# Performance work log

Hardware: AMD Instinct MI355X
Metric: run time of the kernel (lower is better)

Reference implementation:

```python
import jax, jax.numpy as jnp
import numpy as np
from jax import lax

B, SEQ, D, DEPTH = 256, 50, 256, 4
N, K, R = 16, 4, 16  # d_state, d_conv, dt_rank
EPS = 1e-5


def rmsnorm(x, w):
    var = jnp.mean(jnp.square(x), axis=-1, keepdims=True)
    return x * lax.rsqrt(var + EPS) * w


def mamba_mixer(h, in_proj_w, conv_w, conv_b, x_proj_w, dt_proj_w, dt_proj_b, A_log, D_skip, out_proj_w):
    # h: (B, L, D)
    xz = h @ in_proj_w                       # (B, L, 2D)
    x_in, z = jnp.split(xz, 2, axis=-1)      # each (B, L, D)
    # causal depthwise conv1d, kernel K, groups=D
    x_bdl = x_in.transpose(0, 2, 1)          # (B, D, L)
    kern = conv_w[:, None, :]                # (D, 1, K)
    x_c = lax.conv_general_dilated(x_bdl, kern, window_strides=(1,),
                                   padding=[(K - 1, 0)], feature_group_count=D,
                                   dimension_numbers=('NCH', 'OIH', 'NCH'))
    x_c = jax.nn.silu(x_c + conv_b[None, :, None]).transpose(0, 2, 1)  # (B, L, D)
    # input-dependent SSM params
    x_dbl = x_c @ x_proj_w                   # (B, L, R+2N)
    dt = jax.nn.softplus(x_dbl[..., :R] @ dt_proj_w + dt_proj_b)       # (B, L, D)
    Bm = x_dbl[..., R:R + N]                 # (B, L, N)
    Cm = x_dbl[..., R + N:]                  # (B, L, N)
    A = -jnp.exp(A_log)                      # (D, N)
    dA = jnp.exp(dt[..., None] * A)          # (B, L, D, N)
    dBx = (dt * x_c)[..., None] * Bm[:, :, None, :]                    # (B, L, D, N)

    def step(hstate, inp):
        dA_t, dBx_t, C_t = inp
        hstate = dA_t * hstate + dBx_t      # (B, D, N)
        y_t = jnp.einsum('bdn,bn->bd', hstate, C_t)
        return hstate, y_t

    h0 = jnp.zeros((h.shape[0], D, N), dtype=h.dtype)
    xs = (dA.transpose(1, 0, 2, 3), dBx.transpose(1, 0, 2, 3), Cm.transpose(1, 0, 2))
    _, ys = lax.scan(step, h0, xs)           # (L, B, D)
    y = ys.transpose(1, 0, 2) + D_skip * x_c
    y = y * jax.nn.silu(z)
    return y @ out_proj_w                    # (B, L, D)


def setup_inputs() -> dict:
    key = jax.random.key(0)
    ks = jax.random.split(key, 16)
    sc = lambda *s: 0.02
    inp = {
        'x': jax.random.normal(ks[0], (B, SEQ), dtype=jnp.float32),
        'proj_w': jax.random.normal(ks[1], (1, D), dtype=jnp.float32) * 0.5,
        'proj_b': jnp.zeros((D,), dtype=jnp.float32),
        'cls_token': jax.random.normal(ks[2], (1, 1, D), dtype=jnp.float32) * 0.02,
        'pos_embed': jax.random.normal(ks[3], (1, SEQ + 1, D), dtype=jnp.float32) * 0.02,
        'norm_w': jnp.ones((DEPTH, D), dtype=jnp.float32),
        'in_proj_w': jax.random.normal(ks[4], (DEPTH, D, 2 * D), dtype=jnp.float32) * (D ** -0.5),
        'conv_w': jax.random.normal(ks[5], (DEPTH, D, K), dtype=jnp.float32) * 0.3,
        'conv_b': jnp.zeros((DEPTH, D), dtype=jnp.float32),
        'x_proj_w': jax.random.normal(ks[6], (DEPTH, D, R + 2 * N), dtype=jnp.float32) * (D ** -0.5),
        'dt_proj_w': jax.random.normal(ks[7], (DEPTH, R, D), dtype=jnp.float32) * (R ** -0.5),
        'dt_proj_b': jnp.log(jnp.expm1(jnp.full((DEPTH, D), 0.01, dtype=jnp.float32))),
        'A_log': jnp.broadcast_to(jnp.log(jnp.arange(1, N + 1, dtype=jnp.float32)), (DEPTH, D, N)).copy(),
        'D_skip': jnp.ones((DEPTH, D), dtype=jnp.float32),
        'out_proj_w': jax.random.normal(ks[8], (DEPTH, D, D), dtype=jnp.float32) * (D ** -0.5),
        'norm_f_w': jnp.ones((D,), dtype=jnp.float32),
    }
    return inp


def reference(x, proj_w, proj_b, cls_token, pos_embed, norm_w, in_proj_w, conv_w,
              conv_b, x_proj_w, dt_proj_w, dt_proj_b, A_log, D_skip, out_proj_w, norm_f_w):
    # LinearEmbed: (B, SEQ) -> (B, SEQ, 1) -> (B, SEQ, D)
    h = x[..., None] @ proj_w + proj_b
    h = h + pos_embed[:, :-1, :]
    cls = cls_token + pos_embed[:, -1:, :]
    h = jnp.concatenate([jnp.broadcast_to(cls, (h.shape[0], 1, D)), h], axis=1)  # (B, L=51, D)
    residual = None
    for i in range(DEPTH):
        residual = h if residual is None else residual + h
        hn = rmsnorm(residual, norm_w[i])
        h = mamba_mixer(hn, in_proj_w[i], conv_w[i], conv_b[i], x_proj_w[i],
                        dt_proj_w[i], dt_proj_b[i], A_log[i], D_skip[i], out_proj_w[i])
    out = rmsnorm(h, norm_f_w)
    return out[:, 0, :]  # return_type='cls'
```

## Files before the change

kernel.cpp:

```cpp
#include <hip/hip_runtime.h>
#include <math.h>

#define DD 256
#define DEPTH 4
#define XD 48


__global__ __launch_bounds__(256, 1)
void stageA(int L,
            const float* __restrict__ cls_token,
            const float* __restrict__ pos_embed,
            const float* __restrict__ norm_w,
            const float* __restrict__ in_proj_w,
            const float* __restrict__ conv_w,
            const float* __restrict__ conv_b,
            float* __restrict__ ws)
{
    const int tid = threadIdx.x, bid = blockIdx.x;
    float* xc_g = ws;
    float* zv_g = ws + DD;
    const float* hv_g = ws + 2*DD;
    float* res_e = ws + 3*DD;
    float* res_o = ws + 4*DD;

    __shared__ float hn[DD];
    __shared__ float4 part[64][4];
    __shared__ float red[4];
    __shared__ float rstd_s;

    float rn;
    if (L == 0) rn = cls_token[tid] + pos_embed[50*DD + tid];
    else        rn = ((L-1) & 1 ? res_o : res_e)[tid] + hv_g[tid];
    if (bid == 0) ((L & 1) ? res_o : res_e)[tid] = rn;

    float ss = rn * rn;
    #pragma unroll
    for (int o = 32; o > 0; o >>= 1) ss += __shfl_down(ss, o, 64);
    if ((tid & 63) == 0) red[tid >> 6] = ss;
    __syncthreads();
    if (tid == 0)
        rstd_s = rsqrtf((red[0]+red[1]+red[2]+red[3]) * (1.f/DD) + 1e-5f);
    __syncthreads();
    hn[tid] = rn * rstd_s * norm_w[L*DD + tid];
    __syncthreads();

    {
        const float4* W4 = (const float4*)in_proj_w + (size_t)L * DD * 128;
        const int c = tid & 3, seg = tid >> 2;
        const int col4 = bid*4 + c;
        float4 acc = make_float4(0.f, 0.f, 0.f, 0.f);
        #pragma unroll
        for (int i = 0; i < 4; ++i) {
            const int d = seg*4 + i;
            const float h = hn[d];
            const float4 w = W4[(size_t)d*128 + col4];
            acc.x += h*w.x; acc.y += h*w.y; acc.z += h*w.z; acc.w += h*w.w;
        }
        part[seg][c] = acc;
    }
    __syncthreads();
    #pragma unroll
    for (int off = 32; off >= 8; off >>= 1) {
        const int s = tid >> 2, c = tid & 3;
        if (s < off) {
            float4 a = part[s][c], b = part[s+off][c];
            a.x += b.x; a.y += b.y; a.z += b.z; a.w += b.w;
            part[s][c] = a;
        }
        __syncthreads();
    }
    if (tid < 16) {
        const int j = tid;
        float s = 0.f;
        #pragma unroll
        for (int g = 0; g < 8; ++g)
            s += ((const float*)&part[g][j >> 2])[j & 3];
        const int gc = bid*16 + j;
        if (gc < DD) {
            const float pre = conv_w[(L*DD + gc)*4 + 3]*s + conv_b[L*DD + gc];
            xc_g[gc] = pre / (1.f + __expf(-pre));
        } else {
            zv_g[gc - DD] = s;
        }
    }
}

__global__ __launch_bounds__(256, 1)
void stageB(int L,
            const float* __restrict__ x_proj_w,
            const float* __restrict__ dt_proj_w,
            const float* __restrict__ dt_proj_b,
            const float* __restrict__ D_skip,
            const float* __restrict__ out_proj_w,
            float* __restrict__ ws)
{
    const int tid = threadIdx.x, bid = blockIdx.x;
    const float* xc_g = ws;
    const float* zv_g = ws + DD;
    float* hv_g = ws + 2*DD;

    __shared__ float xcl[DD], yv[DD], xdbl[XD];
    __shared__ float xp[XD][4];
    __shared__ float4 part[64][4];

    xcl[tid] = xc_g[tid];
    const float zval = zv_g[tid];
    __syncthreads();

    if (tid < 192) {
        const int j = tid >> 2, q = tid & 3;
        const float* Wx = x_proj_w + (size_t)L * DD * XD;
        float acc = 0.f;
        #pragma unroll 8
        for (int i = 0; i < 64; ++i) {
            const int d = q*64 + i;
            acc += xcl[d] * Wx[(size_t)d*XD + j];
        }
        xp[j][q] = acc;
    }
    __syncthreads();
    if (tid < XD) xdbl[tid] = xp[tid][0] + xp[tid][1] + xp[tid][2] + xp[tid][3];
    __syncthreads();

    {
        const float* Wdt = dt_proj_w + (size_t)L * 16 * DD;
        float acc = dt_proj_b[L*DD + tid];
        #pragma unroll
        for (int r = 0; r < 16; ++r) acc += xdbl[r] * Wdt[r*DD + tid];
        const float dt = fmaxf(acc, 0.f) + log1pf(__expf(-fabsf(acc)));
        float sbc = 0.f;
        #pragma unroll
        for (int n = 0; n < 16; ++n) sbc += xdbl[16+n] * xdbl[32+n];
        const float y = (dt*sbc + D_skip[L*DD + tid]) * xcl[tid];
        yv[tid] = y * (zval / (1.f + __expf(-zval)));
    }
    __syncthreads();

    {
        const float4* Wo = (const float4*)out_proj_w + (size_t)L * DD * 64;
        const int c = tid & 3, seg = tid >> 2;
        const int col4 = bid*4 + c;
        float4 acc = make_float4(0.f, 0.f, 0.f, 0.f);
        #pragma unroll
        for (int i = 0; i < 4; ++i) {
            const int d = seg*4 + i;
            const float y = yv[d];
            const float4 w = Wo[(size_t)d*64 + col4];
            acc.x += y*w.x; acc.y += y*w.y; acc.z += y*w.z; acc.w += y*w.w;
        }
        part[seg][c] = acc;
    }
    __syncthreads();
    #pragma unroll
    for (int off = 32; off >= 8; off >>= 1) {
        const int s = tid >> 2, c = tid & 3;
        if (s < off) {
            float4 a = part[s][c], b = part[s+off][c];
            a.x += b.x; a.y += b.y; a.z += b.z; a.w += b.w;
            part[s][c] = a;
        }
        __syncthreads();
    }
    if (tid < 16) {
        const int j = tid;
        float s = 0.f;
        #pragma unroll
        for (int g = 0; g < 8; ++g)
            s += ((const float*)&part[g][j >> 2])[j & 3];
        hv_g[bid*16 + j] = s;
    }
}

__global__ __launch_bounds__(256, 1)
void finalK(const float* __restrict__ norm_f_w,
            const float* __restrict__ ws,
            float* __restrict__ out)
{
    const int tid = threadIdx.x, bid = blockIdx.x;
    const float* hv_g = ws + 2*DD;
    __shared__ float hn[DD];
    __shared__ float red[4];
    __shared__ float rstd_s;

    const float x = hv_g[tid];
    float ss = x * x;
    #pragma unroll
    for (int o = 32; o > 0; o >>= 1) ss += __shfl_down(ss, o, 64);
    if ((tid & 63) == 0) red[tid >> 6] = ss;
    __syncthreads();
    if (tid == 0)
        rstd_s = rsqrtf((red[0]+red[1]+red[2]+red[3]) * (1.f/DD) + 1e-5f);
    __syncthreads();
    hn[tid] = x * rstd_s * norm_f_w[tid];
    __syncthreads();

    const float4* o4 = (const float4*)hn;
    float4* out4 = (float4*)out;
    #pragma unroll
    for (int k = 0; k < 4; ++k) {
        const int idx = k*256 + tid;
        const int row = bid*16 + (idx >> 6);
        out4[(size_t)row*64 + (idx & 63)] = o4[idx & 63];
    }
}

extern "C" void kernel_launch(void* const* d_in, const int* in_sizes, int n_in,
                              void* d_out, int out_size, void* d_ws, size_t ws_size,
                              hipStream_t stream) {
    const float* cls_token  = (const float*)d_in[3];
    const float* pos_embed  = (const float*)d_in[4];
    const float* norm_w     = (const float*)d_in[5];
    const float* in_proj_w  = (const float*)d_in[6];
    const float* conv_w     = (const float*)d_in[7];
    const float* conv_b     = (const float*)d_in[8];
    const float* x_proj_w   = (const float*)d_in[9];
    const float* dt_proj_w  = (const float*)d_in[10];
    const float* dt_proj_b  = (const float*)d_in[11];
    const float* D_skip     = (const float*)d_in[13];
    const float* out_proj_w = (const float*)d_in[14];
    const float* norm_f_w   = (const float*)d_in[15];
    float* out = (float*)d_out;
    float* ws  = (float*)d_ws;

    for (int L = 0; L < DEPTH; ++L) {
        stageA<<<dim3(32), dim3(256), 0, stream>>>(
            L, cls_token, pos_embed, norm_w, in_proj_w, conv_w, conv_b, ws);
        stageB<<<dim3(16), dim3(256), 0, stream>>>(
            L, x_proj_w, dt_proj_w, dt_proj_b, D_skip, out_proj_w, ws);
    }
    finalK<<<dim3(16), dim3(256), 0, stream>>>(norm_f_w, ws, out);
}
```

Before: 38.12 us.

## Fuse all layer stages into one persistent kernel with grid barriers

Replaces the nine separate kernel launches (two per layer plus a final norm) with a single persistent 16-block kernel. A software grid barrier on an atomic counter separates the phases, and a tiny init kernel resets the counter. Intermediates pass between blocks through agent-scope atomic loads and stores, and the residual now stays in registers. The in_proj stage is retiled so 16 blocks each cover 32 columns. This removes per-launch overhead, but adds spin-barrier latency and relies on relaxed atomics without explicit fences for ordering.

```diff
diff --git a/kernel.cpp b/kernel.cpp
--- a/kernel.cpp
+++ b/kernel.cpp
@@ -4,229 +4,216 @@
 #define DD 256
 #define DEPTH 4
 #define XD 48
-
-
-__global__ __launch_bounds__(256, 1)
-void stageA(int L,
-            const float* __restrict__ cls_token,
-            const float* __restrict__ pos_embed,
-            const float* __restrict__ norm_w,
-            const float* __restrict__ in_proj_w,
-            const float* __restrict__ conv_w,
-            const float* __restrict__ conv_b,
-            float* __restrict__ ws)
+#define NBLK 16
+#define NTHR 256
+
+
+__device__ __forceinline__ float llc_loadf(const float* p) {
+    return __hip_atomic_load(p, __ATOMIC_RELAXED, __HIP_MEMORY_SCOPE_AGENT);
+}
+__device__ __forceinline__ void llc_storef(float* p, float v) {
+    __hip_atomic_store(p, v, __ATOMIC_RELAXED, __HIP_MEMORY_SCOPE_AGENT);
+}
+
+__device__ __forceinline__ void grid_bar(unsigned int* cnt, unsigned int target) {
+    __syncthreads();
+    if (threadIdx.x == 0) {
+        __hip_atomic_fetch_add(cnt, 1u, __ATOMIC_RELAXED, __HIP_MEMORY_SCOPE_AGENT);
+        while (__hip_atomic_load(cnt, __ATOMIC_RELAXED, __HIP_MEMORY_SCOPE_AGENT) < target)
+            __builtin_amdgcn_s_sleep(1);
+    }
+    __syncthreads();
+}
+
+__global__ void netmamba_init(unsigned int* cnt) { *cnt = 0u; }
+
+__global__ __launch_bounds__(NTHR, 1)
+void netmamba_persist(const float* __restrict__ cls_token,
+                      const float* __restrict__ pos_embed,
+                      const float* __restrict__ norm_w,
+                      const float* __restrict__ in_proj_w,
+                      const float* __restrict__ conv_w,
+                      const float* __restrict__ conv_b,
+                      const float* __restrict__ x_proj_w,
+                      const float* __restrict__ dt_proj_w,
+                      const float* __restrict__ dt_proj_b,
+                      const float* __restrict__ D_skip,
+                      const float* __restrict__ out_proj_w,
+                      const float* __restrict__ norm_f_w,
+                      float* __restrict__ out,
+                      float* __restrict__ ws)
 {
     const int tid = threadIdx.x, bid = blockIdx.x;
     float* xc_g = ws;
     float* zv_g = ws + DD;
-    const float* hv_g = ws + 2*DD;
-    float* res_e = ws + 3*DD;
-    float* res_o = ws + 4*DD;
-
-    __shared__ float hn[DD];
-    __shared__ float4 part[64][4];
+    float* hv_g = ws + 2 * DD;
+    unsigned int* cnt = (unsigned int*)(ws + 1024);
+
+    __shared__ float hn[DD], xcl[DD], yv[DD], xdbl[XD];
+    __shared__ float4 partA[32][8];
+    __shared__ float4 partB[64][4];
+    __shared__ float xp[XD][4];
     __shared__ float red[4];
     __shared__ float rstd_s;
 
-    float rn;
-    if (L == 0) rn = cls_token[tid] + pos_embed[50*DD + tid];
-    else        rn = ((L-1) & 1 ? res_o : res_e)[tid] + hv_g[tid];
-    if (bid == 0) ((L & 1) ? res_o : res_e)[tid] = rn;
-
-    float ss = rn * rn;
-    #pragma unroll
-    for (int o = 32; o > 0; o >>= 1) ss += __shfl_down(ss, o, 64);
-    if ((tid & 63) == 0) red[tid >> 6] = ss;
+    float res_reg = 0.f;
+    unsigned int phase = 0;
+
+    for (int L = 0; L < DEPTH; ++L) {
+        float rn;
+        if (L == 0) rn = cls_token[tid] + pos_embed[50 * DD + tid];
+        else        rn = res_reg + llc_loadf(&hv_g[tid]);
+        res_reg = rn;
+
+        float ss = rn * rn;
+        #pragma unroll
+        for (int o = 32; o > 0; o >>= 1) ss += __shfl_down(ss, o, 64);
+        if ((tid & 63) == 0) red[tid >> 6] = ss;
+        __syncthreads();
+        if (tid == 0)
+            rstd_s = rsqrtf((red[0] + red[1] + red[2] + red[3]) * (1.f / DD) + 1e-5f);
+        __syncthreads();
+        hn[tid] = rn * rstd_s * norm_w[L * DD + tid];
+        __syncthreads();
+
+        {
+            const float4* W4 = (const float4*)in_proj_w + (size_t)L * DD * 128;
+            const int cg = tid & 7, seg = tid >> 3;
+            const int col4 = bid * 8 + cg;
+            float4 acc = make_float4(0.f, 0.f, 0.f, 0.f);
+            #pragma unroll
+            for (int i = 0; i < 8; ++i) {
+                const int d = seg * 8 + i;
+                const float h = hn[d];
+                const float4 w = W4[(size_t)d * 128 + col4];
+                acc.x += h * w.x; acc.y += h * w.y;
+                acc.z += h * w.z; acc.w += h * w.w;
+            }
+            partA[seg][cg] = acc;
+        }
+        __syncthreads();
+        if (tid < 32) {
+            const float* pf = (const float*)partA;
+            float s = 0.f;
+            #pragma unroll
+            for (int g = 0; g < 32; ++g) s += pf[g * 32 + tid];
+            const int gc = bid * 32 + tid;
+            if (gc < DD) {
+                const float pre = conv_w[(L * DD + gc) * 4 + 3] * s + conv_b[L * DD + gc];
+                llc_storef(&xc_g[gc], pre / (1.f + __expf(-pre)));
+            } else {
+                llc_storef(&zv_g[gc - DD], s);
+            }
+        }
+        ++phase;
+        grid_bar(cnt, phase * NBLK);
+
+        xcl[tid] = llc_loadf(&xc_g[tid]);
+        const float zval = llc_loadf(&zv_g[tid]);
+        __syncthreads();
+
+        if (tid < 192) {
+            const int j = tid >> 2, q = tid & 3;
+            const float* Wx = x_proj_w + (size_t)L * DD * XD;
+            float acc = 0.f;
+            #pragma unroll 8
+            for (int i = 0; i < 64; ++i) {
+                const int d = q * 64 + i;
+                acc += xcl[d] * Wx[(size_t)d * XD + j];
+            }
+            xp[j][q] = acc;
+        }
+        __syncthreads();
+        if (tid < XD) xdbl[tid] = xp[tid][0] + xp[tid][1] + xp[tid][2] + xp[tid][3];
+        __syncthreads();
+
+        {
+            const float* Wdt = dt_proj_w + (size_t)L * 16 * DD;
+            float acc = dt_proj_b[L * DD + tid];
+            #pragma unroll
+            for (int r = 0; r < 16; ++r) acc += xdbl[r] * Wdt[r * DD + tid];
+            const float dtv = fmaxf(acc, 0.f) + log1pf(__expf(-fabsf(acc)));
+            float sbc = 0.f;
+            #pragma unroll
+            for (int n = 0; n < 16; ++n) sbc += xdbl[16 + n] * xdbl[32 + n];
+            const float y = (dtv * sbc + D_skip[L * DD + tid]) * xcl[tid];
+            yv[tid] = y * (zval / (1.f + __expf(-zval)));
+        }
+        __syncthreads();
+
+        {
+            const float4* Wo = (const float4*)out_proj_w + (size_t)L * DD * 64;
+            const int c = tid & 3, seg = tid >> 2;
+            const int col4 = bid * 4 + c;
+            float4 acc = make_float4(0.f, 0.f, 0.f, 0.f);
+            #pragma unroll
+            for (int i = 0; i < 4; ++i) {
+                const int d = seg * 4 + i;
+                const float y = yv[d];
+                const float4 w = Wo[(size_t)d * 64 + col4];
+                acc.x += y * w.x; acc.y += y * w.y;
+                acc.z += y * w.z; acc.w += y * w.w;
+            }
+            partB[seg][c] = acc;
+        }
+        __syncthreads();
+        #pragma unroll
+        for (int off = 32; off >= 8; off >>= 1) {
+            const int s = tid >> 2, c = tid & 3;
+            if (s < off) {
+                float4 a = partB[s][c], b = partB[s + off][c];
+                a.x += b.x; a.y += b.y; a.z += b.z; a.w += b.w;
+                partB[s][c] = a;
+            }
+            __syncthreads();
+        }
+        if (tid < 16) {
+            const float* pf = (const float*)partB;
+            float s = 0.f;
+            #pragma unroll
+            for (int g = 0; g < 8; ++g) s += pf[g * 16 + tid];
+            llc_storef(&hv_g[bid * 16 + tid], s);
+        }
+        ++phase;
+        grid_bar(cnt, phase * NBLK);
+    }
+
+    {
+        const float x = llc_loadf(&hv_g[tid]);
+        float ss = x * x;
+        #pragma unroll
+        for (int o = 32; o > 0; o >>= 1) ss += __shfl_down(ss, o, 64);
+        if ((tid & 63) == 0) red[tid >> 6] = ss;
+        __syncthreads();
+        if (tid == 0)
+            rstd_s = rsqrtf((red[0] + red[1] + red[2] + red[3]) * (1.f / DD) + 1e-5f);
+        __syncthreads();
+        hn[tid] = x * rstd_s * norm_f_w[tid];
+    }
     __syncthreads();
-    if (tid == 0)
-        rstd_s = rsqrtf((red[0]+red[1]+red[2]+red[3]) * (1.f/DD) + 1e-5f);
-    __syncthreads();
-    hn[tid] = rn * rstd_s * norm_w[L*DD + tid];
-    __syncthreads();
-
     {
-        const float4* W4 = (const float4*)in_proj_w + (size_t)L * DD * 128;
-        const int c = tid & 3, seg = tid >> 2;
-        const int col4 = bid*4 + c;
-        float4 acc = make_float4(0.f, 0.f, 0.f, 0.f);
-        #pragma unroll
-        for (int i = 0; i < 4; ++i) {
-            const int d = seg*4 + i;
-            const float h = hn[d];
-            const float4 w = W4[(size_t)d*128 + col4];
-            acc.x += h*w.x; acc.y += h*w.y; acc.z += h*w.z; acc.w += h*w.w;
-        }
-        part[seg][c] = acc;
-    }
-    __syncthreads();
-    #pragma unroll
-    for (int off = 32; off >= 8; off >>= 1) {
-        const int s = tid >> 2, c = tid & 3;
-        if (s < off) {
-            float4 a = part[s][c], b = part[s+off][c];
-            a.x += b.x; a.y += b.y; a.z += b.z; a.w += b.w;
-            part[s][c] = a;
-        }
-        __syncthreads();
-    }
-    if (tid < 16) {
-        const int j = tid;
-        float s = 0.f;
-        #pragma unroll
-        for (int g = 0; g < 8; ++g)
-            s += ((const float*)&part[g][j >> 2])[j & 3];
-        const int gc = bid*16 + j;
-        if (gc < DD) {
-            const float pre = conv_w[(L*DD + gc)*4 + 3]*s + conv_b[L*DD + gc];
-            xc_g[gc] = pre / (1.f + __expf(-pre));
-        } else {
-            zv_g[gc - DD] = s;
-        }
-    }
-}
-
-__global__ __launch_bounds__(256, 1)
-void stageB(int L,
-            const float* __restrict__ x_proj_w,
-            const float* __restrict__ dt_proj_w,
-            const float* __restrict__ dt_proj_b,
-            const float* __restrict__ D_skip,
-            const float* __restrict__ out_proj_w,
-            float* __restrict__ ws)
-{
-    const int tid = threadIdx.x, bid = blockIdx.x;
-    const float* xc_g = ws;
-    const float* zv_g = ws + DD;
-    float* hv_g = ws + 2*DD;
-
-    __shared__ float xcl[DD], yv[DD], xdbl[XD];
-    __shared__ float xp[XD][4];
-    __shared__ float4 part[64][4];
-
-    xcl[tid] = xc_g[tid];
-    const float zval = zv_g[tid];
-    __syncthreads();
-
-    if (tid < 192) {
-        const int j = tid >> 2, q = tid & 3;
-        const float* Wx = x_proj_w + (size_t)L * DD * XD;
-        float acc = 0.f;
-        #pragma unroll 8
-        for (int i = 0; i < 64; ++i) {
-            const int d = q*64 + i;
-            acc += xcl[d] * Wx[(size_t)d*XD + j];
-        }
-        xp[j][q] = acc;
-    }
-    __syncthreads();
-    if (tid < XD) xdbl[tid] = xp[tid][0] + xp[tid][1] + xp[tid][2] + xp[tid][3];
-    __syncthreads();
-
-    {
-        const float* Wdt = dt_proj_w + (size_t)L * 16 * DD;
-        float acc = dt_proj_b[L*DD + tid];
-        #pragma unroll
-        for (int r = 0; r < 16; ++r) acc += xdbl[r] * Wdt[r*DD + tid];
-        const float dt = fmaxf(acc, 0.f) + log1pf(__expf(-fabsf(acc)));
-        float sbc = 0.f;
-        #pragma unroll
-        for (int n = 0; n < 16; ++n) sbc += xdbl[16+n] * xdbl[32+n];
-        const float y = (dt*sbc + D_skip[L*DD + tid]) * xcl[tid];
-        yv[tid] = y * (zval / (1.f + __expf(-zval)));
-    }
-    __syncthreads();
-
-    {
-        const float4* Wo = (const float4*)out_proj_w + (size_t)L * DD * 64;
-        const int c = tid & 3, seg = tid >> 2;
-        const int col4 = bid*4 + c;
-        float4 acc = make_float4(0.f, 0.f, 0.f, 0.f);
-        #pragma unroll
-        for (int i = 0; i < 4; ++i) {
-            const int d = seg*4 + i;
-            const float y = yv[d];
-            const float4 w = Wo[(size_t)d*64 + col4];
-            acc.x += y*w.x; acc.y += y*w.y; acc.z += y*w.z; acc.w += y*w.w;
-        }
-        part[seg][c] = acc;
-    }
-    __syncthreads();
-    #pragma unroll
-    for (int off = 32; off >= 8; off >>= 1) {
-        const int s = tid >> 2, c = tid & 3;
-        if (s < off) {
-            float4 a = part[s][c], b = part[s+off][c];
-            a.x += b.x; a.y += b.y; a.z += b.z; a.w += b.w;
-            part[s][c] = a;
-        }
-        __syncthreads();
-    }
-    if (tid < 16) {
-        const int j = tid;
-        float s = 0.f;
-        #pragma unroll
-        for (int g = 0; g < 8; ++g)
-            s += ((const float*)&part[g][j >> 2])[j & 3];
-        hv_g[bid*16 + j] = s;
-    }
-}
-
-__global__ __launch_bounds__(256, 1)
-void finalK(const float* __restrict__ norm_f_w,
-            const float* __restrict__ ws,
-            float* __restrict__ out)
-{
-    const int tid = threadIdx.x, bid = blockIdx.x;
-    const float* hv_g = ws + 2*DD;
-    __shared__ float hn[DD];
-    __shared__ float red[4];
-    __shared__ float rstd_s;
-
-    const float x = hv_g[tid];
-    float ss = x * x;
-    #pragma unroll
-    for (int o = 32; o > 0; o >>= 1) ss += __shfl_down(ss, o, 64);
-    if ((tid & 63) == 0) red[tid >> 6] = ss;
-    __syncthreads();
-    if (tid == 0)
-        rstd_s = rsqrtf((red[0]+red[1]+red[2]+red[3]) * (1.f/DD) + 1e-5f);
-    __syncthreads();
-    hn[tid] = x * rstd_s * norm_f_w[tid];
-    __syncthreads();
-
-    const float4* o4 = (const float4*)hn;
-    float4* out4 = (float4*)out;
-    #pragma unroll
-    for (int k = 0; k < 4; ++k) {
-        const int idx = k*256 + tid;
-        const int row = bid*16 + (idx >> 6);
-        out4[(size_t)row*64 + (idx & 63)] = o4[idx & 63];
+        const float4* o4 = (const float4*)hn;
+        float4* out4 = (float4*)out;
+        #pragma unroll
+        for (int k = 0; k < 4; ++k) {
+            const int idx = k * NTHR + tid;
+            const int row = bid * 16 + (idx >> 6);
+            out4[(size_t)row * 64 + (idx & 63)] = o4[idx & 63];
+        }
     }
 }
 
 extern "C" void kernel_launch(void* const* d_in, const int* in_sizes, int n_in,
                               void* d_out, int out_size, void* d_ws, size_t ws_size,
                               hipStream_t stream) {
-    const float* cls_token  = (const float*)d_in[3];
-    const float* pos_embed  = (const float*)d_in[4];
-    const float* norm_w     = (const float*)d_in[5];
-    const float* in_proj_w  = (const float*)d_in[6];
-    const float* conv_w     = (const float*)d_in[7];
-    const float* conv_b     = (const float*)d_in[8];
-    const float* x_proj_w   = (const float*)d_in[9];
-    const float* dt_proj_w  = (const float*)d_in[10];
-    const float* dt_proj_b  = (const float*)d_in[11];
-    const float* D_skip     = (const float*)d_in[13];
-    const float* out_proj_w = (const float*)d_in[14];
-    const float* norm_f_w   = (const float*)d_in[15];
-    float* out = (float*)d_out;
-    float* ws  = (float*)d_ws;
-
-    for (int L = 0; L < DEPTH; ++L) {
-        stageA<<<dim3(32), dim3(256), 0, stream>>>(
-            L, cls_token, pos_embed, norm_w, in_proj_w, conv_w, conv_b, ws);
-        stageB<<<dim3(16), dim3(256), 0, stream>>>(
-            L, x_proj_w, dt_proj_w, dt_proj_b, D_skip, out_proj_w, ws);
-    }
-    finalK<<<dim3(16), dim3(256), 0, stream>>>(norm_f_w, ws, out);
-}
+    float* ws = (float*)d_ws;
+    unsigned int* cnt = (unsigned int*)(ws + 1024);
+
+    netmamba_init<<<dim3(1), dim3(1), 0, stream>>>(cnt);
+    netmamba_persist<<<dim3(NBLK), dim3(NTHR), 0, stream>>>(
+        (const float*)d_in[3], (const float*)d_in[4], (const float*)d_in[5],
+        (const float*)d_in[6], (const float*)d_in[7], (const float*)d_in[8],
+        (const float*)d_in[9], (const float*)d_in[10], (const float*)d_in[11],
+        (const float*)d_in[13], (const float*)d_in[14], (const float*)d_in[15],
+        (float*)d_out, ws);
+}
```

Measured after the change: 44.11 us. +15.7%, slower.
